# Kernel optimization log

Measured on AMD Instinct MI355X. Metric: run time of the kernel, lower is better.

## Reference

```python
import jax, jax.numpy as jnp
import numpy as np

B, T, J, D = 64, 2048, 128, 256

def setup_inputs() -> dict:
    key = jax.random.key(0)
    k1, k2, k3 = jax.random.split(key, 3)
    H = jax.random.normal(k1, (B, T, D), dtype=jnp.float32)
    U = jax.random.normal(k2, (B, J, D), dtype=jnp.float32)
    w = jax.random.normal(k3, (3 * D, 1), dtype=jnp.float32) * 0.05
    return {"H": H, "U": U, "w": w}


def reference(H, U, w):
    # Original: tile H to (B,T,J,D), tile U to (B,T,J,D), concat [H,U,H*U] -> (B,T,J,3D),
    # then dot with w (3D,1) and squeeze -> (B,T,J).
    # Equivalent trilinear form without materializing the tiled tensor:
    # S[b,t,j] = H[b,t]@w1 + U[b,j]@w2 + (H[b,t]*w3)@U[b,j]
    d = H.shape[-1]
    wv = w[:, 0]
    w1, w2, w3 = wv[:d], wv[d:2 * d], wv[2 * d:]
    s_h = jnp.einsum('btd,d->bt', H, w1)          # (B,T)
    s_u = jnp.einsum('bjd,d->bj', U, w2)          # (B,J)
    s_hu = jnp.einsum('btd,bjd->btj', H * w3, U)  # (B,T,J)
    return s_h[:, :, None] + s_u[:, None, :] + s_hu
```

## Files before the change

### kernel.cpp

```cpp
#include <hip/hip_runtime.h>
#include <stdint.h>

#define Bb 64
#define Tt 2048
#define Jj 128
#define Dd 256


typedef __attribute__((ext_vector_type(8))) __bf16 bf16x8;
typedef __attribute__((ext_vector_type(8))) unsigned short ushort8v;
typedef __attribute__((ext_vector_type(4))) float f32x4;

__device__ __forceinline__ unsigned short f2bf(float f) {
    unsigned int u = __builtin_bit_cast(unsigned int, f);
    u += 0x7FFFu + ((u >> 16) & 1u);
    return (unsigned short)(u >> 16);
}

__device__ __forceinline__ bf16x8 pack8(const float4& a0, const float4& a1) {
    bf16x8 r;
    r[0] = (__bf16)a0.x; r[1] = (__bf16)a0.y; r[2] = (__bf16)a0.z; r[3] = (__bf16)a0.w;
    r[4] = (__bf16)a1.x; r[5] = (__bf16)a1.y; r[6] = (__bf16)a1.z; r[7] = (__bf16)a1.w;
    return r;
}

__global__ __launch_bounds__(256)
void prep_all(const float* __restrict__ U, const float* __restrict__ w,
              unsigned short* __restrict__ Up, float* __restrict__ su) {
    const int bid = blockIdx.x;
    const int tid = threadIdx.x;
    if (bid < 1152) {
        const int idx = bid * 256 + tid;
        const int b   = idx / 4608;
        const int rem = idx - b * 4608;
        const int j   = rem >> 9;
        const int ks  = (rem >> 6) & 7;
        const int l   = idx & 63;
        const int k0  = ks * 32 + (l >> 4) * 8;

        ushort8v s;
        if (j < 8) {
            const int row = j * 16 + (l & 15);
            const float* up = U + ((size_t)(b * Jj + row)) * Dd + k0;
            const float* wp = w + 2 * Dd + k0;
            const float4 u0 = *(const float4*)(up);
            const float4 u1 = *(const float4*)(up + 4);
            const float4 w0 = *(const float4*)(wp);
            const float4 w1 = *(const float4*)(wp + 4);
            s[0] = f2bf(u0.x * w0.x); s[1] = f2bf(u0.y * w0.y);
            s[2] = f2bf(u0.z * w0.z); s[3] = f2bf(u0.w * w0.w);
            s[4] = f2bf(u1.x * w1.x); s[5] = f2bf(u1.y * w1.y);
            s[6] = f2bf(u1.z * w1.z); s[7] = f2bf(u1.w * w1.w);
        } else {
            const bool n0 = (l & 15) == 0;
#pragma unroll
            for (int e = 0; e < 8; ++e)
                s[e] = n0 ? f2bf(w[k0 + e]) : (unsigned short)0;
        }
        ((ushort8v*)Up)[idx] = s;
    } else {
        const int row  = (bid - 1152) * 4 + (tid >> 6);
        const int lane = tid & 63;
        const float4 u = *(const float4*)(U + (size_t)row * Dd + lane * 4);
        const float4 v = *(const float4*)(w + Dd + lane * 4);
        float s = u.x * v.x + u.y * v.y + u.z * v.z + u.w * v.w;
#pragma unroll
        for (int d = 1; d < 64; d <<= 1) s += __shfl_xor(s, d);
        if (lane == 0) su[row] = s;
    }
}

__global__ __launch_bounds__(512, 4)
void sim_main(const float* __restrict__ H, const unsigned short* __restrict__ Up,
              const float* __restrict__ su, float* __restrict__ out) {
    __shared__ ushort8v lUp[4608];

    const int tid   = threadIdx.x;
    const int wid   = tid >> 6;
    const int lane  = tid & 63;
    const int row16 = lane & 15;
    const int quad  = lane >> 4;

    const int b  = blockIdx.x >> 4;
    const int m0 = (blockIdx.x & 15) * 128 + wid * 16;

    const ushort8v* Ub = (const ushort8v*)Up + (size_t)b * 9 * 512;
#pragma unroll
    for (int p = 0; p < 9; ++p)
        lUp[tid + p * 512] = Ub[tid + p * 512];

    const float* Hp = H + ((size_t)(b * Tt + m0 + row16)) * Dd + quad * 8;
    float4 hb0[3], hb1[3];
#pragma unroll
    for (int p = 0; p < 3; ++p) {
        hb0[p] = *(const float4*)(Hp + p * 32);
        hb1[p] = *(const float4*)(Hp + p * 32 + 4);
    }

    f32x4 acc[9];
#pragma unroll
    for (int j = 0; j < 9; ++j) acc[j] = (f32x4){0.f, 0.f, 0.f, 0.f};

    __syncthreads();

#pragma unroll
    for (int ks = 0; ks < 8; ++ks) {
        const int slot = ks % 3;
        const float4 h0 = hb0[slot];
        const float4 h1 = hb1[slot];
        if (ks < 5) {
            hb0[slot] = *(const float4*)(Hp + (ks + 3) * 32);
            hb1[slot] = *(const float4*)(Hp + (ks + 3) * 32 + 4);
        }

        const bf16x8 af = pack8(h0, h1);
#pragma unroll
        for (int j = 0; j < 9; ++j) {
            const bf16x8 bf = __builtin_bit_cast(bf16x8, lUp[(j * 8 + ks) * 64 + lane]);
            acc[j] = __builtin_amdgcn_mfma_f32_16x16x32_bf16(af, bf, acc[j], 0, 0, 0);
        }
    }

    float shv[4];
#pragma unroll
    for (int rg = 0; rg < 4; ++rg)
        shv[rg] = __shfl(acc[8][rg], quad * 16);

    float* outW = out + ((size_t)(b * Tt + m0)) * Jj;
    const float* sub = su + b * Jj;
#pragma unroll
    for (int j = 0; j < 8; ++j) {
        const int col = j * 16 + row16;
        const float suv = sub[col];
#pragma unroll
        for (int rg = 0; rg < 4; ++rg)
            outW[(size_t)(quad * 4 + rg) * Jj + col] = acc[j][rg] + shv[rg] + suv;
    }
}

extern "C" void kernel_launch(void* const* d_in, const int* in_sizes, int n_in,
                              void* d_out, int out_size, void* d_ws, size_t ws_size,
                              hipStream_t stream) {
    const float* H = (const float*)d_in[0];
    const float* U = (const float*)d_in[1];
    const float* w = (const float*)d_in[2];
    float* out = (float*)d_out;

    unsigned short* Up = (unsigned short*)d_ws;
    float* su = (float*)((char*)d_ws + (size_t)Bb * 9 * 512 * 16);

    prep_all<<<3200, 256, 0, stream>>>(U, w, Up, su);
    sim_main<<<Bb * 16, 512, 0, stream>>>(H, Up, su, out);
}
```

Measured before the change: 234.9 us.

## Fuse U preprocessing and s_u reduction into the main MFMA kernel

```diff
diff --git a/kernel.cpp b/kernel.cpp
--- a/kernel.cpp
+++ b/kernel.cpp
@@ -24,24 +24,37 @@
     return r;
 }
 
-__global__ __launch_bounds__(256)
-void prep_all(const float* __restrict__ U, const float* __restrict__ w,
-              unsigned short* __restrict__ Up, float* __restrict__ su) {
-    const int bid = blockIdx.x;
-    const int tid = threadIdx.x;
-    if (bid < 1152) {
-        const int idx = bid * 256 + tid;
-        const int b   = idx / 4608;
-        const int rem = idx - b * 4608;
-        const int j   = rem >> 9;
-        const int ks  = (rem >> 6) & 7;
-        const int l   = idx & 63;
-        const int k0  = ks * 32 + (l >> 4) * 8;
+__global__ __launch_bounds__(512, 4)
+void sim_fused(const float* __restrict__ H, const float* __restrict__ U,
+               const float* __restrict__ w, float* __restrict__ out) {
+    __shared__ ushort8v lUp[4608];
+    __shared__ float lsu[Jj];
 
+    const int tid   = threadIdx.x;
+    const int wid   = tid >> 6;
+    const int lane  = tid & 63;
+    const int row16 = lane & 15;
+    const int quad  = lane >> 4;
+
+    const int b  = blockIdx.x >> 4;
+    const int m0 = (blockIdx.x & 15) * 128 + wid * 16;
+
+    const float* Hp = H + ((size_t)(b * Tt + m0 + row16)) * Dd + quad * 8;
+    float4 hb0[3], hb1[3];
+#pragma unroll
+    for (int p = 0; p < 3; ++p) {
+        hb0[p] = *(const float4*)(Hp + p * 32);
+        hb1[p] = *(const float4*)(Hp + p * 32 + 4);
+    }
+
+    const float* Ubase = U + (size_t)b * Jj * Dd;
+    const int k0 = wid * 32 + quad * 8;
+#pragma unroll
+    for (int p = 0; p < 9; ++p) {
         ushort8v s;
-        if (j < 8) {
-            const int row = j * 16 + (l & 15);
-            const float* up = U + ((size_t)(b * Jj + row)) * Dd + k0;
+        if (p < 8) {
+            const int row = p * 16 + row16;
+            const float* up = Ubase + (size_t)row * Dd + k0;
             const float* wp = w + 2 * Dd + k0;
             const float4 u0 = *(const float4*)(up);
             const float4 u1 = *(const float4*)(up + 4);
@@ -52,49 +65,29 @@
             s[4] = f2bf(u1.x * w1.x); s[5] = f2bf(u1.y * w1.y);
             s[6] = f2bf(u1.z * w1.z); s[7] = f2bf(u1.w * w1.w);
         } else {
-            const bool n0 = (l & 15) == 0;
+            const bool n0 = row16 == 0;
 #pragma unroll
             for (int e = 0; e < 8; ++e)
                 s[e] = n0 ? f2bf(w[k0 + e]) : (unsigned short)0;
         }
-        ((ushort8v*)Up)[idx] = s;
-    } else {
-        const int row  = (bid - 1152) * 4 + (tid >> 6);
-        const int lane = tid & 63;
-        const float4 u = *(const float4*)(U + (size_t)row * Dd + lane * 4);
-        const float4 v = *(const float4*)(w + Dd + lane * 4);
-        float s = u.x * v.x + u.y * v.y + u.z * v.z + u.w * v.w;
+        lUp[(p * 8 + wid) * 64 + lane] = s;
+    }
+
+    {
+        const int row = tid >> 2;
+        const int c0  = (tid & 3) * 64;
+        const float* up = Ubase + (size_t)row * Dd + c0;
+        const float* wp = w + Dd + c0;
+        float ssum = 0.f;
 #pragma unroll
-        for (int d = 1; d < 64; d <<= 1) s += __shfl_xor(s, d);
-        if (lane == 0) su[row] = s;
-    }
-}
-
-__global__ __launch_bounds__(512, 4)
-void sim_main(const float* __restrict__ H, const unsigned short* __restrict__ Up,
-              const float* __restrict__ su, float* __restrict__ out) {
-    __shared__ ushort8v lUp[4608];
-
-    const int tid   = threadIdx.x;
-    const int wid   = tid >> 6;
-    const int lane  = tid & 63;
-    const int row16 = lane & 15;
-    const int quad  = lane >> 4;
-
-    const int b  = blockIdx.x >> 4;
-    const int m0 = (blockIdx.x & 15) * 128 + wid * 16;
-
-    const ushort8v* Ub = (const ushort8v*)Up + (size_t)b * 9 * 512;
-#pragma unroll
-    for (int p = 0; p < 9; ++p)
-        lUp[tid + p * 512] = Ub[tid + p * 512];
-
-    const float* Hp = H + ((size_t)(b * Tt + m0 + row16)) * Dd + quad * 8;
-    float4 hb0[3], hb1[3];
-#pragma unroll
-    for (int p = 0; p < 3; ++p) {
-        hb0[p] = *(const float4*)(Hp + p * 32);
-        hb1[p] = *(const float4*)(Hp + p * 32 + 4);
+        for (int i = 0; i < 16; ++i) {
+            const float4 u = *(const float4*)(up + i * 4);
+            const float4 v = *(const float4*)(wp + i * 4);
+            ssum += u.x * v.x + u.y * v.y + u.z * v.z + u.w * v.w;
+        }
+        ssum += __shfl_xor(ssum, 1);
+        ssum += __shfl_xor(ssum, 2);
+        if ((tid & 3) == 0) lsu[row] = ssum;
     }
 
     f32x4 acc[9];
@@ -127,11 +120,10 @@
         shv[rg] = __shfl(acc[8][rg], quad * 16);
 
     float* outW = out + ((size_t)(b * Tt + m0)) * Jj;
-    const float* sub = su + b * Jj;
 #pragma unroll
     for (int j = 0; j < 8; ++j) {
         const int col = j * 16 + row16;
-        const float suv = sub[col];
+        const float suv = lsu[col];
 #pragma unroll
         for (int rg = 0; rg < 4; ++rg)
             outW[(size_t)(quad * 4 + rg) * Jj + col] = acc[j][rg] + shv[rg] + suv;
@@ -145,10 +137,7 @@
     const float* U = (const float*)d_in[1];
     const float* w = (const float*)d_in[2];
     float* out = (float*)d_out;
+    (void)d_ws; (void)ws_size;
 
-    unsigned short* Up = (unsigned short*)d_ws;
-    float* su = (float*)((char*)d_ws + (size_t)Bb * 9 * 512 * 16);
-
-    prep_all<<<3200, 256, 0, stream>>>(U, w, Up, su);
-    sim_main<<<Bb * 16, 512, 0, stream>>>(H, Up, su, out);
+    sim_fused<<<Bb * 16, 512, 0, stream>>>(H, U, w, out);
 }
```

Measured after the change: 244.0 us. 3.8% more time.
